# Kernel tuning notes

Hardware: AMD Instinct MI355X
Metric: run time of the kernel (lower is better)

Reference implementation:

```python
import jax, jax.numpy as jnp
import numpy as np

B, S, T, D = 32, 128, 65536, 768
VOCAB, N_SEC, N_TEMP, N_NEG, MAX_SENT, N_TS = 30522, 6, 3, 2, 128, 512
LN_EPS = 1e-5


def setup_inputs() -> dict:
    key = jax.random.key(0)
    ks = jax.random.split(key, 16)
    return {
        "token_ids": jax.random.randint(ks[0], (T,), 0, VOCAB),
        "segment_ids": jnp.sort(jax.random.randint(ks[1], (T,), 0, B * S)),
        "section_ids": jax.random.randint(ks[2], (B, S), 0, N_SEC),
        "temporality_ids": jax.random.randint(ks[3], (B, S), 0, N_TEMP),
        "negation_ids": jax.random.randint(ks[4], (B, S), 0, N_NEG),
        "position_ids": jax.random.randint(ks[5], (B, S), 0, MAX_SENT),
        "timestamp_ids": jax.random.randint(ks[6], (B, S), 0, N_TS),
        "token_table": jax.random.normal(ks[7], (VOCAB, D), jnp.float32),
        "section_table": jax.random.normal(ks[8], (N_SEC, D), jnp.float32),
        "temporality_table": jax.random.normal(ks[9], (N_TEMP, D), jnp.float32),
        "negation_table": jax.random.normal(ks[10], (N_NEG, D), jnp.float32),
        "position_table": jax.random.normal(ks[11], (MAX_SENT, D), jnp.float32),
        "timestamp_table": jax.random.normal(ks[12], (N_TS, D), jnp.float32),
        "ln_gamma": jnp.ones((D,), jnp.float32),
        "ln_beta": jnp.zeros((D,), jnp.float32),
        "proj_w": jax.random.normal(ks[13], (D, D), jnp.float32) * (1.0 / np.sqrt(D)),
        "proj_b": jnp.zeros((D,), jnp.float32),
    }


def reference(token_ids, segment_ids, section_ids, temporality_ids, negation_ids,
              position_ids, timestamp_ids, token_table, section_table,
              temporality_table, negation_table, position_table, timestamp_table,
              ln_gamma, ln_beta, proj_w, proj_b):
    # ragged per-sentence token-embedding mean pool (segment mean over B*S slots)
    tok = token_table[token_ids]                                  # [T, D]
    sums = jax.ops.segment_sum(tok, segment_ids, num_segments=B * S)
    cnt = jax.ops.segment_sum(jnp.ones((T,), tok.dtype), segment_ids,
                              num_segments=B * S)
    base = (sums / jnp.maximum(cnt, 1.0)[:, None]).reshape(B, S, D)
    # multi-embedding sum
    enriched = (base
                + section_table[section_ids]
                + temporality_table[temporality_ids]
                + negation_table[negation_ids]
                + position_table[position_ids]
                + timestamp_table[timestamp_ids])                 # [B, S, D]
    # LayerNorm + Linear
    mu = enriched.mean(-1, keepdims=True)
    var = jnp.mean(jnp.square(enriched - mu), axis=-1, keepdims=True)
    normed = (enriched - mu) * jax.lax.rsqrt(var + LN_EPS) * ln_gamma + ln_beta
    tokens = jnp.einsum('bsd,ed->bse', normed, proj_w) + proj_b   # [B, S, D]
    padding_mask = jnp.zeros((B, S), dtype=bool)                  # all sentences valid
    return tokens, padding_mask
```

## Files before the change

kernel.cpp:

```cpp
#include <hip/hip_runtime.h>
#include <stdint.h>

#define Tn 65536
#define Dn 768
#define NSEG 4096

typedef __bf16 bf16;
typedef __bf16 bf16x8 __attribute__((ext_vector_type(8)));
typedef float f32x4 __attribute__((ext_vector_type(4)));

__device__ inline void f4add(float4& a, const float4& v) {
  a.x += v.x; a.y += v.y; a.z += v.z; a.w += v.w;
}

__global__ __launch_bounds__(256) void k_prep(
    const float* __restrict__ w, bf16* __restrict__ wb,
    float* __restrict__ mask_out,
    const int* __restrict__ seg, int* __restrict__ starts)
{
  const int b = blockIdx.x;
  if (b < 576) {
    const int i = b * 256 + threadIdx.x;
    const float4 v = ((const float4*)w)[i];
    alignas(8) bf16 o[4] = {(bf16)v.x, (bf16)v.y, (bf16)v.z, (bf16)v.w};
    ((ushort4*)wb)[i] = *(ushort4*)o;
  } else if (b < 592) {
    mask_out[(b - 576) * 256 + threadIdx.x] = 0.0f;
  } else {
    const int t = (b - 592) * 256 + threadIdx.x;
    const int s = seg[t];
    const int sp = (t == 0) ? -1 : seg[t - 1];
    for (int k = sp + 1; k <= s; ++k) starts[k] = t;
    if (t == Tn - 1)
      for (int k = s + 1; k <= NSEG; ++k) starts[k] = Tn;
  }
}

__global__ void k_pool_ln(
    const int* __restrict__ token_ids, const int* __restrict__ starts,
    const int* __restrict__ section_ids, const int* __restrict__ temporality_ids,
    const int* __restrict__ negation_ids, const int* __restrict__ position_ids,
    const int* __restrict__ timestamp_ids,
    const float* __restrict__ token_table, const float* __restrict__ section_table,
    const float* __restrict__ temporality_table, const float* __restrict__ negation_table,
    const float* __restrict__ position_table, const float* __restrict__ timestamp_table,
    const float* __restrict__ gamma, const float* __restrict__ beta,
    bf16* __restrict__ out_normed)
{
  const int n = blockIdx.x;
  const int lane = threadIdx.x;
  const int start = starts[n];
  const int end   = starts[n + 1];
  const float scale = 1.0f / fmaxf((float)(end - start), 1.0f);

  const float4* tt = (const float4*)token_table;

  const float4* e1 = (const float4*)(section_table     + (size_t)section_ids[n]     * Dn);
  const float4* e2 = (const float4*)(temporality_table + (size_t)temporality_ids[n] * Dn);
  const float4* e3 = (const float4*)(negation_table    + (size_t)negation_ids[n]    * Dn);
  const float4* e4 = (const float4*)(position_table    + (size_t)position_ids[n]    * Dn);
  const float4* e5 = (const float4*)(timestamp_table   + (size_t)timestamp_ids[n]   * Dn);
  float4 en[3];
  #pragma unroll
  for (int j = 0; j < 3; ++j) {
    const int d = j * 64 + lane;
    float4 q = e1[d];
    f4add(q, e2[d]); f4add(q, e3[d]); f4add(q, e4[d]); f4add(q, e5[d]);
    en[j] = q;
  }

  float4 acc[3];
  #pragma unroll
  for (int j = 0; j < 3; ++j) acc[j] = make_float4(0.f, 0.f, 0.f, 0.f);

  int t = start;
  int ids[8];
  #pragma unroll
  for (int u = 0; u < 8; ++u)
    ids[u] = token_ids[(t + u < Tn) ? t + u : Tn - 1];

  while (t + 8 <= end) {
    float4 L[8][3];
    #pragma unroll
    for (int u = 0; u < 8; ++u) {
      const float4* r = tt + (size_t)ids[u] * 192;
      #pragma unroll
      for (int j = 0; j < 3; ++j) L[u][j] = r[j * 64 + lane];
    }
    t += 8;
    #pragma unroll
    for (int u = 0; u < 8; ++u)
      ids[u] = token_ids[(t + u < Tn) ? t + u : Tn - 1];
    #pragma unroll
    for (int j = 0; j < 3; ++j) {
      f4add(L[0][j], L[1][j]); f4add(L[2][j], L[3][j]);
      f4add(L[4][j], L[5][j]); f4add(L[6][j], L[7][j]);
      f4add(L[0][j], L[2][j]); f4add(L[4][j], L[6][j]);
      f4add(L[0][j], L[4][j]); f4add(acc[j], L[0][j]);
    }
  }
  for (int u = 0; t < end; ++t, ++u) {
    const float4* r = tt + (size_t)ids[u] * 192;
    #pragma unroll
    for (int j = 0; j < 3; ++j) f4add(acc[j], r[j * 64 + lane]);
  }

  float4 e[3];
  #pragma unroll
  for (int j = 0; j < 3; ++j) {
    e[j].x = acc[j].x * scale + en[j].x;
    e[j].y = acc[j].y * scale + en[j].y;
    e[j].z = acc[j].z * scale + en[j].z;
    e[j].w = acc[j].w * scale + en[j].w;
  }

  float s = 0.f;
  #pragma unroll
  for (int j = 0; j < 3; ++j) s += e[j].x + e[j].y + e[j].z + e[j].w;
  #pragma unroll
  for (int o = 32; o > 0; o >>= 1) s += __shfl_xor(s, o, 64);
  const float mu = s * (1.0f / 768.0f);

  float v = 0.f;
  #pragma unroll
  for (int j = 0; j < 3; ++j) {
    e[j].x -= mu; e[j].y -= mu; e[j].z -= mu; e[j].w -= mu;
    v += e[j].x * e[j].x + e[j].y * e[j].y + e[j].z * e[j].z + e[j].w * e[j].w;
  }
  #pragma unroll
  for (int o = 32; o > 0; o >>= 1) v += __shfl_xor(v, o, 64);
  const float inv = rsqrtf(v * (1.0f / 768.0f) + 1e-5f);

  #pragma unroll
  for (int j = 0; j < 3; ++j) {
    const int d = j * 64 + lane;
    const float4 g = ((const float4*)gamma)[d];
    const float4 b = ((const float4*)beta)[d];
    alignas(8) bf16 o[4];
    o[0] = (bf16)(e[j].x * inv * g.x + b.x);
    o[1] = (bf16)(e[j].y * inv * g.y + b.y);
    o[2] = (bf16)(e[j].z * inv * g.z + b.z);
    o[3] = (bf16)(e[j].w * inv * g.w + b.w);
    *(ushort4*)(out_normed + (size_t)n * Dn + 4 * d) = *(ushort4*)o;
  }
}

__global__ __launch_bounds__(256) void k_gemm(
    const bf16* __restrict__ A, const bf16* __restrict__ W,
    const float* __restrict__ bias, float* __restrict__ out)
{
  __shared__ bf16 As[64 * 32];
  __shared__ bf16 Bs[128 * 32];
  const int tid  = threadIdx.x;
  const int lane = tid & 63;
  const int w    = tid >> 6;
  const int m0 = blockIdx.y * 64;
  const int n0 = blockIdx.x * 128;
  const int wm = (w >> 1) * 32;
  const int wn = (w & 1) * 64;

  f32x4 acc[2][4];
  #pragma unroll
  for (int i = 0; i < 2; ++i)
    #pragma unroll
    for (int j = 0; j < 4; ++j) acc[i][j] = (f32x4){0.f, 0.f, 0.f, 0.f};

  const int fr = tid >> 2;
  const int fc = (tid & 3) * 8;
  const bf16* agp = A + (size_t)(m0 + fr) * 768 + fc;
  const bf16* bgp = W + (size_t)(n0 + fr) * 768 + fc;

  for (int kt = 0; kt < 24; ++kt) {
    __syncthreads();
    __builtin_amdgcn_global_load_lds(
        (const __attribute__((address_space(1))) void*)(agp + kt * 32),
        (__attribute__((address_space(3))) void*)(As + tid * 8), 16, 0, 0);
    #pragma unroll
    for (int it = 0; it < 2; ++it) {
      const int f = it * 256 + tid;
      __builtin_amdgcn_global_load_lds(
          (const __attribute__((address_space(1))) void*)(bgp + (size_t)it * 64 * 768 + kt * 32),
          (__attribute__((address_space(3))) void*)(Bs + f * 8), 16, 0, 0);
    }
    __syncthreads();

    bf16x8 af[2], bfr[4];
    #pragma unroll
    for (int i = 0; i < 2; ++i)
      af[i] = *(const bf16x8*)(As + (wm + i * 16 + (lane & 15)) * 32 + (lane >> 4) * 8);
    #pragma unroll
    for (int j = 0; j < 4; ++j)
      bfr[j] = *(const bf16x8*)(Bs + (wn + j * 16 + (lane & 15)) * 32 + (lane >> 4) * 8);

    #pragma unroll
    for (int i = 0; i < 2; ++i)
      #pragma unroll
      for (int j = 0; j < 4; ++j)
        acc[i][j] = __builtin_amdgcn_mfma_f32_16x16x32_bf16(af[i], bfr[j], acc[i][j], 0, 0, 0);
  }

  float bvals[4];
  #pragma unroll
  for (int j = 0; j < 4; ++j) bvals[j] = bias[n0 + wn + j * 16 + (lane & 15)];
  const int r0 = (lane >> 4) * 4;
  #pragma unroll
  for (int i = 0; i < 2; ++i) {
    #pragma unroll
    for (int r = 0; r < 4; ++r) {
      const int gm = m0 + wm + i * 16 + r0 + r;
      float* orow = out + (size_t)gm * 768 + n0 + wn;
      #pragma unroll
      for (int j = 0; j < 4; ++j)
        orow[j * 16 + (lane & 15)] = acc[i][j][r] + bvals[j];
    }
  }
}

extern "C" void kernel_launch(void* const* d_in, const int* in_sizes, int n_in,
                              void* d_out, int out_size, void* d_ws, size_t ws_size,
                              hipStream_t stream) {
  const int* token_ids       = (const int*)d_in[0];
  const int* segment_ids     = (const int*)d_in[1];
  const int* section_ids     = (const int*)d_in[2];
  const int* temporality_ids = (const int*)d_in[3];
  const int* negation_ids    = (const int*)d_in[4];
  const int* position_ids    = (const int*)d_in[5];
  const int* timestamp_ids   = (const int*)d_in[6];
  const float* token_table       = (const float*)d_in[7];
  const float* section_table     = (const float*)d_in[8];
  const float* temporality_table = (const float*)d_in[9];
  const float* negation_table    = (const float*)d_in[10];
  const float* position_table    = (const float*)d_in[11];
  const float* timestamp_table   = (const float*)d_in[12];
  const float* ln_gamma = (const float*)d_in[13];
  const float* ln_beta  = (const float*)d_in[14];
  const float* proj_w   = (const float*)d_in[15];
  const float* proj_b   = (const float*)d_in[16];

  float* out = (float*)d_out;
  bf16* wsW = (bf16*)d_ws;
  bf16* wsN = wsW + (size_t)Dn * Dn;
  int*  wsS = (int*)((char*)d_ws + (size_t)(Dn * Dn + NSEG * Dn) * 2);

  k_prep<<<848, 256, 0, stream>>>(proj_w, wsW, out + (size_t)NSEG * Dn,
                                  segment_ids, wsS);
  k_pool_ln<<<NSEG, 64, 0, stream>>>(token_ids, wsS, section_ids,
      temporality_ids, negation_ids, position_ids, timestamp_ids,
      token_table, section_table, temporality_table, negation_table,
      position_table, timestamp_table, ln_gamma, ln_beta, wsN);
  k_gemm<<<dim3(6, 64), 256, 0, stream>>>(wsN, wsW, proj_b, out);
}
```

Before: 202.2 us.

## Move weight cast into pool kernel and enlarge GEMM M tile to 128

The weight bf16 conversion and the mask zeroing move out of the prep kernel into extra blocks of the pooling kernel, so the prep kernel only computes segment starts. The GEMM tile grows from 64x128 to 128x128, with each wave computing a 64x64 sub-tile using 4x4 MFMA accumulators. This cuts redundant weight loads and raises MFMA work per shared-memory load. The trade-off is that the grid shrinks to 192 blocks, which may underfill the 256 CUs, and register use per wave rises.

```diff
diff --git a/kernel.cpp b/kernel.cpp
--- a/kernel.cpp
+++ b/kernel.cpp
@@ -4,6 +4,8 @@
 #define Tn 65536
 #define Dn 768
 #define NSEG 4096
+#define NWBLK 576
+#define NMBLK 16
 
 typedef __bf16 bf16;
 typedef __bf16 bf16x8 __attribute__((ext_vector_type(8)));
@@ -14,26 +16,14 @@
 }
 
 __global__ __launch_bounds__(256) void k_prep(
-    const float* __restrict__ w, bf16* __restrict__ wb,
-    float* __restrict__ mask_out,
     const int* __restrict__ seg, int* __restrict__ starts)
 {
-  const int b = blockIdx.x;
-  if (b < 576) {
-    const int i = b * 256 + threadIdx.x;
-    const float4 v = ((const float4*)w)[i];
-    alignas(8) bf16 o[4] = {(bf16)v.x, (bf16)v.y, (bf16)v.z, (bf16)v.w};
-    ((ushort4*)wb)[i] = *(ushort4*)o;
-  } else if (b < 592) {
-    mask_out[(b - 576) * 256 + threadIdx.x] = 0.0f;
-  } else {
-    const int t = (b - 592) * 256 + threadIdx.x;
-    const int s = seg[t];
-    const int sp = (t == 0) ? -1 : seg[t - 1];
-    for (int k = sp + 1; k <= s; ++k) starts[k] = t;
-    if (t == Tn - 1)
-      for (int k = s + 1; k <= NSEG; ++k) starts[k] = Tn;
-  }
+  const int t = blockIdx.x * 256 + threadIdx.x;
+  const int s = seg[t];
+  const int sp = (t == 0) ? -1 : seg[t - 1];
+  for (int k = sp + 1; k <= s; ++k) starts[k] = t;
+  if (t == Tn - 1)
+    for (int k = s + 1; k <= NSEG; ++k) starts[k] = Tn;
 }
 
 __global__ void k_pool_ln(
@@ -45,10 +35,29 @@
     const float* __restrict__ temporality_table, const float* __restrict__ negation_table,
     const float* __restrict__ position_table, const float* __restrict__ timestamp_table,
     const float* __restrict__ gamma, const float* __restrict__ beta,
-    bf16* __restrict__ out_normed)
+    bf16* __restrict__ out_normed,
+    const float* __restrict__ proj_w, bf16* __restrict__ wb,
+    float* __restrict__ mask_out)
 {
   const int n = blockIdx.x;
   const int lane = threadIdx.x;
+
+  if (n >= NSEG) {
+    if (n < NSEG + NWBLK) {
+      const int base = ((n - NSEG) * 64 + lane) * 4;
+      #pragma unroll
+      for (int u = 0; u < 4; ++u) {
+        const float4 v = ((const float4*)proj_w)[base + u];
+        alignas(8) bf16 o[4] = {(bf16)v.x, (bf16)v.y, (bf16)v.z, (bf16)v.w};
+        ((ushort4*)wb)[base + u] = *(ushort4*)o;
+      }
+    } else {
+      ((float4*)mask_out)[(n - NSEG - NWBLK) * 64 + lane] =
+          make_float4(0.f, 0.f, 0.f, 0.f);
+    }
+    return;
+  }
+
   const int start = starts[n];
   const int end   = starts[n + 1];
   const float scale = 1.0f / fmaxf((float)(end - start), 1.0f);
@@ -149,51 +158,56 @@
     const bf16* __restrict__ A, const bf16* __restrict__ W,
     const float* __restrict__ bias, float* __restrict__ out)
 {
-  __shared__ bf16 As[64 * 32];
+  __shared__ bf16 As[128 * 32];
   __shared__ bf16 Bs[128 * 32];
   const int tid  = threadIdx.x;
   const int lane = tid & 63;
   const int w    = tid >> 6;
-  const int m0 = blockIdx.y * 64;
+  const int m0 = blockIdx.y * 128;
   const int n0 = blockIdx.x * 128;
-  const int wm = (w >> 1) * 32;
+  const int wm = (w >> 1) * 64;
   const int wn = (w & 1) * 64;
 
-  f32x4 acc[2][4];
-  #pragma unroll
-  for (int i = 0; i < 2; ++i)
+  f32x4 acc[4][4];
+  #pragma unroll
+  for (int i = 0; i < 4; ++i)
     #pragma unroll
     for (int j = 0; j < 4; ++j) acc[i][j] = (f32x4){0.f, 0.f, 0.f, 0.f};
 
-  const int fr = tid >> 2;
-  const int fc = (tid & 3) * 8;
-  const bf16* agp = A + (size_t)(m0 + fr) * 768 + fc;
-  const bf16* bgp = W + (size_t)(n0 + fr) * 768 + fc;
+  const int sr = tid >> 2;
+  const int sc = (tid & 3) * 8;
+  const bf16* a0 = A + (size_t)(m0 + sr) * 768 + sc;
+  const bf16* a1 = a0 + (size_t)64 * 768;
+  const bf16* b0 = W + (size_t)(n0 + sr) * 768 + sc;
+  const bf16* b1 = b0 + (size_t)64 * 768;
 
   for (int kt = 0; kt < 24; ++kt) {
+    const int ko = kt * 32;
     __syncthreads();
     __builtin_amdgcn_global_load_lds(
-        (const __attribute__((address_space(1))) void*)(agp + kt * 32),
+        (const __attribute__((address_space(1))) void*)(a0 + ko),
         (__attribute__((address_space(3))) void*)(As + tid * 8), 16, 0, 0);
-    #pragma unroll
-    for (int it = 0; it < 2; ++it) {
-      const int f = it * 256 + tid;
-      __builtin_amdgcn_global_load_lds(
-          (const __attribute__((address_space(1))) void*)(bgp + (size_t)it * 64 * 768 + kt * 32),
-          (__attribute__((address_space(3))) void*)(Bs + f * 8), 16, 0, 0);
-    }
+    __builtin_amdgcn_global_load_lds(
+        (const __attribute__((address_space(1))) void*)(a1 + ko),
+        (__attribute__((address_space(3))) void*)(As + (256 + tid) * 8), 16, 0, 0);
+    __builtin_amdgcn_global_load_lds(
+        (const __attribute__((address_space(1))) void*)(b0 + ko),
+        (__attribute__((address_space(3))) void*)(Bs + tid * 8), 16, 0, 0);
+    __builtin_amdgcn_global_load_lds(
+        (const __attribute__((address_space(1))) void*)(b1 + ko),
+        (__attribute__((address_space(3))) void*)(Bs + (256 + tid) * 8), 16, 0, 0);
     __syncthreads();
 
-    bf16x8 af[2], bfr[4];
-    #pragma unroll
-    for (int i = 0; i < 2; ++i)
+    bf16x8 af[4], bfr[4];
+    #pragma unroll
+    for (int i = 0; i < 4; ++i)
       af[i] = *(const bf16x8*)(As + (wm + i * 16 + (lane & 15)) * 32 + (lane >> 4) * 8);
     #pragma unroll
     for (int j = 0; j < 4; ++j)
       bfr[j] = *(const bf16x8*)(Bs + (wn + j * 16 + (lane & 15)) * 32 + (lane >> 4) * 8);
 
     #pragma unroll
-    for (int i = 0; i < 2; ++i)
+    for (int i = 0; i < 4; ++i)
       #pragma unroll
       for (int j = 0; j < 4; ++j)
         acc[i][j] = __builtin_amdgcn_mfma_f32_16x16x32_bf16(af[i], bfr[j], acc[i][j], 0, 0, 0);
@@ -204,7 +218,7 @@
   for (int j = 0; j < 4; ++j) bvals[j] = bias[n0 + wn + j * 16 + (lane & 15)];
   const int r0 = (lane >> 4) * 4;
   #pragma unroll
-  for (int i = 0; i < 2; ++i) {
+  for (int i = 0; i < 4; ++i) {
     #pragma unroll
     for (int r = 0; r < 4; ++r) {
       const int gm = m0 + wm + i * 16 + r0 + r;
@@ -242,11 +256,11 @@
   bf16* wsN = wsW + (size_t)Dn * Dn;
   int*  wsS = (int*)((char*)d_ws + (size_t)(Dn * Dn + NSEG * Dn) * 2);
 
-  k_prep<<<848, 256, 0, stream>>>(proj_w, wsW, out + (size_t)NSEG * Dn,
-                                  segment_ids, wsS);
-  k_pool_ln<<<NSEG, 64, 0, stream>>>(token_ids, wsS, section_ids,
+  k_prep<<<256, 256, 0, stream>>>(segment_ids, wsS);
+  k_pool_ln<<<NSEG + NWBLK + NMBLK, 64, 0, stream>>>(token_ids, wsS, section_ids,
       temporality_ids, negation_ids, position_ids, timestamp_ids,
       token_table, section_table, temporality_table, negation_table,
-      position_table, timestamp_table, ln_gamma, ln_beta, wsN);
-  k_gemm<<<dim3(6, 64), 256, 0, stream>>>(wsN, wsW, proj_b, out);
-}
+      position_table, timestamp_table, ln_gamma, ln_beta, wsN,
+      proj_w, wsW, out + (size_t)NSEG * Dn);
+  k_gemm<<<dim3(6, 32), 256, 0, stream>>>(wsN, wsW, proj_b, out);
+}
```

Measured after the change: 204.7 us. No clear change (+1.2%).
